# Kernel optimization log

Hardware: AMD Instinct MI355X
Metric: run time of the kernel (lower is better)

Reference implementation:

```python
import jax, jax.numpy as jnp
import numpy as np

HEADS = 16
D_MODEL = 1024


def setup_inputs() -> dict:
    key = jax.random.key(0)
    ks = jax.random.split(key, 12)
    B, S, D = 4, 2048, D_MODEL
    s = 1.0 / np.sqrt(D)
    return {
        "q": jax.random.normal(ks[0], (B, S, D), jnp.float32),
        "k": jax.random.normal(ks[1], (B, S, D), jnp.float32),
        "v": jax.random.normal(ks[2], (B, S, D), jnp.float32),
        "mask": jnp.ones((B, S, S), jnp.int32),
        "W_q": jax.random.normal(ks[3], (D, D), jnp.float32) * s,
        "b_q": jnp.zeros((D,), jnp.float32),
        "W_k": jax.random.normal(ks[4], (D, D), jnp.float32) * s,
        "b_k": jnp.zeros((D,), jnp.float32),
        "W_v": jax.random.normal(ks[5], (D, D), jnp.float32) * s,
        "b_v": jnp.zeros((D,), jnp.float32),
        "W_o": jax.random.normal(ks[6], (D, D), jnp.float32) * s,
        "b_o": jnp.zeros((D,), jnp.float32),
    }


def reference(q, k, v, mask, W_q, b_q, W_k, b_k, W_v, b_v, W_o, b_o):
    B, Sq, D = q.shape
    H = HEADS
    d_k = D // H
    # torch Linear: x @ W.T + b
    qh = (q @ W_q.T + b_q).reshape(B, Sq, H, d_k).transpose(0, 2, 1, 3)
    kh = (k @ W_k.T + b_k).reshape(B, -1, H, d_k).transpose(0, 2, 1, 3)
    vh = (v @ W_v.T + b_v).reshape(B, -1, H, d_k).transpose(0, 2, 1, 3)
    scores = jnp.einsum("bhqd,bhkd->bhqk", qh, kh) / jnp.sqrt(jnp.float32(d_k))
    scores = jnp.where(mask[:, None, :, :] == 0, -jnp.inf, scores)
    attn = jax.nn.softmax(scores, axis=-1)
    out = jnp.einsum("bhqk,bhkd->bhqd", attn, vh)
    out = out.transpose(0, 2, 1, 3).reshape(B, Sq, D)
    return out @ W_o.T + b_o
```

## Files before the change

### kernel.cpp

```cpp
#include <hip/hip_runtime.h>
#include <hip/hip_bf16.h>
#include <cmath>
#include <cstddef>

#define B_  4
#define S_  2048
#define D_  1024
#define H_  16
#define DK_ 64
#define M_  (B_*S_)
#define MB(x) ((size_t)(x) << 20)

typedef unsigned short u16;
typedef __attribute__((ext_vector_type(8))) short s16x8;
typedef __attribute__((ext_vector_type(8))) unsigned short u16x8;
typedef __attribute__((ext_vector_type(4))) unsigned short u16x4;
typedef __attribute__((ext_vector_type(4))) float f32x4;
typedef __attribute__((ext_vector_type(4))) unsigned int u32x4;
typedef __attribute__((ext_vector_type(2))) unsigned long long ull2;

typedef __attribute__((address_space(3))) char as3char;
typedef __attribute__((address_space(1))) const char as1char;

__device__ inline u16 f2bf(float f) {
  unsigned int u = __float_as_uint(f);
  u += 0x7fffu + ((u >> 16) & 1u);
  return (u16)(u >> 16);
}
__device__ inline float bf2f(u16 h) {
  return __uint_as_float(((unsigned int)h) << 16);
}

__device__ inline size_t tsw(int m, int k) {
  int row = m & 127, kk = k & 63;
  return ((size_t)((m >> 7) * 16 + (k >> 6)) << 14)
       + (size_t)(((row * 128 + (kk >> 3) * 16) ^ ((row & 7) << 4)) + (kk & 7) * 2);
}

__global__ __launch_bounds__(256)
void pack_mask(const int* __restrict__ mask, unsigned long long* __restrict__ Mp)
{
  int w    = blockIdx.x * 4 + (threadIdx.x >> 6);
  int lane = threadIdx.x & 63;
  int m = mask[(size_t)w * 64 + lane];
  unsigned long long bits = __ballot(m != 0);
  if (lane == 0) Mp[w] = bits;
}

__global__ __launch_bounds__(256)
void split_w_t(const float* __restrict__ W, u16* __restrict__ hi,
               u16* __restrict__ lo)
{
  int id = blockIdx.x * 256 + threadIdx.x;
  int n  = id >> 7;
  int k8 = (id & 127) << 3;
  const float* p = W + (size_t)n * 1024 + k8;
  float4 x0 = *(const float4*)p;
  float4 x1 = *(const float4*)(p + 4);
  float xs[8] = {x0.x, x0.y, x0.z, x0.w, x1.x, x1.y, x1.z, x1.w};
  u16x8 h, l;
#pragma unroll
  for (int e = 0; e < 8; ++e) {
    u16 hh = f2bf(xs[e]);
    h[e] = hh;
    l[e] = f2bf(xs[e] - bf2f(hh));
  }
  size_t byte = tsw(n, k8);
  *(u16x8*)((char*)hi + byte) = h;
  *(u16x8*)((char*)lo + byte) = l;
}

__global__ __launch_bounds__(256)
void cvt3(const float* __restrict__ a, const float* __restrict__ b,
          const float* __restrict__ c, u16* __restrict__ oa,
          u16* __restrict__ ob, u16* __restrict__ oc)
{
  const float* src = blockIdx.z == 0 ? a : (blockIdx.z == 1 ? b : c);
  u16*         dst = blockIdx.z == 0 ? oa : (blockIdx.z == 1 ? ob : oc);
  int id = blockIdx.x * 256 + threadIdx.x;
  int m  = id >> 7;
  int k8 = (id & 127) << 3;
  const float* p = src + (size_t)m * 1024 + k8;
  float4 x0 = *(const float4*)p;
  float4 x1 = *(const float4*)(p + 4);
  u16x8 px;
  px[0]=f2bf(x0.x); px[1]=f2bf(x0.y); px[2]=f2bf(x0.z); px[3]=f2bf(x0.w);
  px[4]=f2bf(x1.x); px[5]=f2bf(x1.y); px[6]=f2bf(x1.z); px[7]=f2bf(x1.w);
  *(u16x8*)((char*)dst + tsw(m, k8)) = px;
}

template<int MODE>
__global__ __launch_bounds__(256)
void proj_gemm_t(const u16* __restrict__ Xb, const u16* __restrict__ Wb,
                 const float* __restrict__ bias, u16* __restrict__ out,
                 float scale)
{
  __shared__ __align__(16) u16 smem[16384];
  char* const sX = (char*)smem;
  char* const sW = (char*)smem + 16384;

  const int tid  = threadIdx.x;
  const int lane = tid & 63, wid = tid >> 6;
  const int l15  = lane & 15, l4 = lane >> 4;
  const int wm = (wid >> 1) * 64, wn = (wid & 1) * 64;
  const int mb = blockIdx.x, nb = blockIdx.y;

  f32x4 acc[4][4];
#pragma unroll
  for (int i = 0; i < 4; ++i)
#pragma unroll
    for (int j = 0; j < 4; ++j)
      acc[i][j] = f32x4{0.f, 0.f, 0.f, 0.f};

  const char* xsrc = (const char*)Xb + ((size_t)(mb * 16) << 14) + wid * 4096 + lane * 16;
  const char* wsrc = (const char*)Wb + ((size_t)(nb * 16) << 14) + wid * 4096 + lane * 16;

  for (int kb = 0; kb < 16; ++kb) {
#pragma unroll
    for (int i = 0; i < 4; ++i) {
      __builtin_amdgcn_global_load_lds((const as1char*)(xsrc + i * 1024),
                                       (as3char*)(sX + wid * 4096 + i * 1024), 16, 0, 0);
      __builtin_amdgcn_global_load_lds((const as1char*)(wsrc + i * 1024),
                                       (as3char*)(sW + wid * 4096 + i * 1024), 16, 0, 0);
    }
    xsrc += 16384; wsrc += 16384;
    __syncthreads();

#pragma unroll
    for (int kc = 0; kc < 2; ++kc) {
      s16x8 af[4], bf[4];
#pragma unroll
      for (int i = 0; i < 4; ++i) {
        int ar = wm + i * 16 + l15;
        af[i] = *(const s16x8*)(sX + ((ar * 128 + kc * 64 + l4 * 16) ^ ((ar & 7) << 4)));
        int br = wn + i * 16 + l15;
        bf[i] = *(const s16x8*)(sW + ((br * 128 + kc * 64 + l4 * 16) ^ ((br & 7) << 4)));
      }
#pragma unroll
      for (int i = 0; i < 4; ++i)
#pragma unroll
        for (int j = 0; j < 4; ++j)
          acc[i][j] = __builtin_amdgcn_mfma_f32_16x16x32_bf16(af[i], bf[j], acc[i][j], 0, 0, 0);
    }
    __syncthreads();
  }

  float bj[4];
#pragma unroll
  for (int j = 0; j < 4; ++j) bj[j] = bias[nb * 128 + wn + j * 16 + l15];

#pragma unroll
  for (int i = 0; i < 4; ++i) {
#pragma unroll
    for (int r = 0; r < 4; ++r) {
      int mm = mb * 128 + wm + i * 16 + l4 * 4 + r;
      int bb = mm >> 11, s = mm & (S_ - 1);
#pragma unroll
      for (int j = 0; j < 4; ++j) {
        int n = nb * 128 + wn + j * 16 + l15;
        int hh = n >> 6, d = n & 63;
        u16 val = f2bf((acc[i][j][r] + bj[j]) * scale);
        if (MODE == 0)
          out[(((size_t)bb * H_ + hh) * S_ + s) * DK_ + d] = val;
        else
          out[(((size_t)bb * H_ + hh) * DK_ + d) * S_ + s] = val;
      }
    }
  }
}

__global__ __launch_bounds__(256)
void proj_out_t(const u16* __restrict__ Xhi, const u16* __restrict__ Xlo,
                const u16* __restrict__ Whi, const u16* __restrict__ Wlo,
                const float* __restrict__ bias, float* __restrict__ out)
{
  __shared__ __align__(16) u16 smem[32768];
  char* const sXh = (char*)smem;
  char* const sXl = (char*)smem + 16384;
  char* const sWh = (char*)smem + 32768;
  char* const sWl = (char*)smem + 49152;

  const int tid  = threadIdx.x;
  const int lane = tid & 63, wid = tid >> 6;
  const int l15  = lane & 15, l4 = lane >> 4;
  const int wm = (wid >> 1) * 64, wn = (wid & 1) * 64;
  const int mb = blockIdx.x, nb = blockIdx.y;

  f32x4 acc[4][4];
#pragma unroll
  for (int i = 0; i < 4; ++i)
#pragma unroll
    for (int j = 0; j < 4; ++j)
      acc[i][j] = f32x4{0.f, 0.f, 0.f, 0.f};

  const int toff = wid * 4096 + lane * 16;
  const char* xh = (const char*)Xhi + ((size_t)(mb * 16) << 14) + toff;
  const char* xl = (const char*)Xlo + ((size_t)(mb * 16) << 14) + toff;
  const char* wh = (const char*)Whi + ((size_t)(nb * 16) << 14) + toff;
  const char* wl = (const char*)Wlo + ((size_t)(nb * 16) << 14) + toff;

  for (int kb = 0; kb < 16; ++kb) {
#pragma unroll
    for (int i = 0; i < 4; ++i) {
      __builtin_amdgcn_global_load_lds((const as1char*)(xh + i * 1024),
                                       (as3char*)(sXh + wid * 4096 + i * 1024), 16, 0, 0);
      __builtin_amdgcn_global_load_lds((const as1char*)(xl + i * 1024),
                                       (as3char*)(sXl + wid * 4096 + i * 1024), 16, 0, 0);
      __builtin_amdgcn_global_load_lds((const as1char*)(wh + i * 1024),
                                       (as3char*)(sWh + wid * 4096 + i * 1024), 16, 0, 0);
      __builtin_amdgcn_global_load_lds((const as1char*)(wl + i * 1024),
                                       (as3char*)(sWl + wid * 4096 + i * 1024), 16, 0, 0);
    }
    xh += 16384; xl += 16384; wh += 16384; wl += 16384;
    __syncthreads();

#pragma unroll
    for (int kc = 0; kc < 2; ++kc) {
      s16x8 ah[4], al[4], bh[4], bl[4];
#pragma unroll
      for (int i = 0; i < 4; ++i) {
        int ar = wm + i * 16 + l15;
        int aoff = (ar * 128 + kc * 64 + l4 * 16) ^ ((ar & 7) << 4);
        ah[i] = *(const s16x8*)(sXh + aoff);
        al[i] = *(const s16x8*)(sXl + aoff);
        int br = wn + i * 16 + l15;
        int boff = (br * 128 + kc * 64 + l4 * 16) ^ ((br & 7) << 4);
        bh[i] = *(const s16x8*)(sWh + boff);
        bl[i] = *(const s16x8*)(sWl + boff);
      }
#pragma unroll
      for (int i = 0; i < 4; ++i)
#pragma unroll
        for (int j = 0; j < 4; ++j) {
          acc[i][j] = __builtin_amdgcn_mfma_f32_16x16x32_bf16(ah[i], bh[j], acc[i][j], 0, 0, 0);
          acc[i][j] = __builtin_amdgcn_mfma_f32_16x16x32_bf16(ah[i], bl[j], acc[i][j], 0, 0, 0);
          acc[i][j] = __builtin_amdgcn_mfma_f32_16x16x32_bf16(al[i], bh[j], acc[i][j], 0, 0, 0);
        }
    }
    __syncthreads();
  }

  float bj[4];
#pragma unroll
  for (int j = 0; j < 4; ++j) bj[j] = bias[nb * 128 + wn + j * 16 + l15];

#pragma unroll
  for (int i = 0; i < 4; ++i) {
#pragma unroll
    for (int r = 0; r < 4; ++r) {
      int mm = mb * 128 + wm + i * 16 + l4 * 4 + r;
#pragma unroll
      for (int j = 0; j < 4; ++j) {
        int n = nb * 128 + wn + j * 16 + l15;
        out[(size_t)mm * D_ + n] = acc[i][j][r] + bj[j];
      }
    }
  }
}

__global__ __launch_bounds__(512)
void flash_attn_mfma5(const u16* __restrict__ Qh, const u16* __restrict__ Kh,
                      const u16* __restrict__ Vt,
                      const unsigned long long* __restrict__ Mp,
                      u16* __restrict__ AOhi, u16* __restrict__ AOlo)
{
  __shared__ __align__(16) char smem[16896];
  char* const sK = smem;
  char* const sV = smem + 8192;

  const int tid  = threadIdx.x;
  const int lane = tid & 63, wid = tid >> 6;
  const int l15  = lane & 15, l4 = lane >> 4;

  const int bh = blockIdx.y;
  const int b  = bh >> 4, h = bh & 15;
  const int q0 = blockIdx.x * 128;
  const int qw = q0 + wid * 16;
  const int myq = qw + l15;

  const float L2E = 1.4426950408889634f;

  const u16* qbase = Qh + ((size_t)bh * S_ + myq) * DK_;
  s16x8 qf[2];
  qf[0] = *(const s16x8*)(qbase + l4 * 8);
  qf[1] = *(const s16x8*)(qbase + 32 + l4 * 8);

  const int srow = tid >> 3;
  const int sd8  = (tid & 7) * 8;
  const int kdst = (srow * 128 + (tid & 7) * 16) ^ ((srow & 7) << 4);
  const int vdst = srow * 136 + (((tid & 7) * 16) ^ (((srow >> 3) & 7) << 4));
  const u16* kg = Kh + (size_t)bh * S_ * DK_ + (size_t)srow * DK_ + sd8;
  const u16* vg = Vt + (size_t)bh * DK_ * S_ + (size_t)srow * S_ + sd8;

  const int kswz = (l15 & 7) << 4;
  const int kcol = l4 * 16;

  const unsigned long long* mrow = Mp + ((size_t)b * S_ + myq) * (S_ / 64);

  f32x4 o[4];
#pragma unroll
  for (int n = 0; n < 4; ++n) o[n] = f32x4{0.f, 0.f, 0.f, 0.f};
  float m_i = -INFINITY, l_i = 0.f;
  float ml2 = -1e30f * L2E;

  u16x8 kreg = *(const u16x8*)(kg);
  u16x8 vreg = *(const u16x8*)(vg);
  unsigned long long mb_next = mrow[0];

  for (int t = 0; t < S_ / 64; ++t) {
    __syncthreads();
    *(u16x8*)(sK + kdst) = kreg;
    *(u16x8*)(sV + vdst) = vreg;
    unsigned long long mbits = mb_next;
    __syncthreads();

    if (t + 1 < S_ / 64) {
      kreg = *(const u16x8*)(kg + (size_t)(t + 1) * 64 * DK_);
      vreg = *(const u16x8*)(vg + (size_t)(t + 1) * 64);
      mb_next = mrow[t + 1];
    }

    f32x4 sc[4];
#pragma unroll
    for (int n = 0; n < 4; ++n) {
      sc[n] = f32x4{0.f, 0.f, 0.f, 0.f};
#pragma unroll
      for (int kc = 0; kc < 2; ++kc) {
        int row = n * 16 + l15;
        s16x8 kf = *(const s16x8*)(sK + ((row * 128 + kc * 64 + kcol) ^ kswz));
        sc[n] = __builtin_amdgcn_mfma_f32_16x16x32_bf16(kf, qf[kc], sc[n], 0, 0, 0);
      }
    }

    float s[4][4];
    if (__all(mbits == 0xFFFFFFFFFFFFFFFFull)) {
#pragma unroll
      for (int n = 0; n < 4; ++n)
#pragma unroll
        for (int r = 0; r < 4; ++r) s[n][r] = sc[n][r];
    } else {
#pragma unroll
      for (int n = 0; n < 4; ++n) {
        unsigned mb2 = (unsigned)(mbits >> (n * 16 + l4 * 4)) & 15u;
#pragma unroll
        for (int r = 0; r < 4; ++r)
          s[n][r] = (mb2 >> r) & 1u ? sc[n][r] : -INFINITY;
      }
    }

    float mt = fmaxf(fmaxf(s[0][0], s[0][1]), fmaxf(s[0][2], s[0][3]));
#pragma unroll
    for (int n = 1; n < 4; ++n)
      mt = fmaxf(mt, fmaxf(fmaxf(s[n][0], s[n][1]), fmaxf(s[n][2], s[n][3])));
    mt = fmaxf(mt, __shfl_xor(mt, 16));
    mt = fmaxf(mt, __shfl_xor(mt, 32));

    if (!__all(mt - m_i <= 8.f)) {
      float mn = fmaxf(m_i, mt);
      float alpha = (m_i == -INFINITY) ? 0.f
                    : __builtin_amdgcn_exp2f((m_i - mn) * L2E);
      float ab[4];
#pragma unroll
      for (int r = 0; r < 4; ++r) ab[r] = __shfl(alpha, l4 * 4 + r);
#pragma unroll
      for (int n = 0; n < 4; ++n)
#pragma unroll
        for (int r = 0; r < 4; ++r) o[n][r] *= ab[r];
      l_i *= alpha;
      m_i = mn;
      ml2 = fmaxf(mn, -1e30f) * L2E;
    }

    float p[4][4];
    float rs = 0.f;
#pragma unroll
    for (int n = 0; n < 4; ++n)
#pragma unroll
      for (int r = 0; r < 4; ++r) {
        p[n][r] = __builtin_amdgcn_exp2f(fmaf(s[n][r], L2E, -ml2));
        rs += p[n][r];
      }
    rs += __shfl_xor(rs, 16);
    rs += __shfl_xor(rs, 32);
    l_i += rs;

    s16x8 pf[2];
#pragma unroll
    for (int kc = 0; kc < 2; ++kc) {
      unsigned r0, r1, r2, r3;
      asm("v_cvt_pk_bf16_f32 %0, %1, %2" : "=v"(r0) : "v"(p[2*kc][0]),   "v"(p[2*kc][1]));
      asm("v_cvt_pk_bf16_f32 %0, %1, %2" : "=v"(r1) : "v"(p[2*kc][2]),   "v"(p[2*kc][3]));
      asm("v_cvt_pk_bf16_f32 %0, %1, %2" : "=v"(r2) : "v"(p[2*kc+1][0]), "v"(p[2*kc+1][1]));
      asm("v_cvt_pk_bf16_f32 %0, %1, %2" : "=v"(r3) : "v"(p[2*kc+1][2]), "v"(p[2*kc+1][3]));
      u32x4 uu = {r0, r1, r2, r3};
      pf[kc] = __builtin_bit_cast(s16x8, uu);
    }

#pragma unroll
    for (int kc = 0; kc < 2; ++kc) {
      int k0b = kc * 64 + 8 * l4;
#pragma unroll
      for (int n = 0; n < 4; ++n) {
        int d    = n * 16 + l15;
        int rowb = d * 136;
        int swz  = ((d >> 3) & 7) << 4;
        ull2 uu;
        uu[0] = *(const unsigned long long*)(sV + rowb + (k0b ^ swz));
        uu[1] = *(const unsigned long long*)(sV + rowb + ((k0b + 32) ^ swz));
        s16x8 vf = __builtin_bit_cast(s16x8, uu);
        o[n] = __builtin_amdgcn_mfma_f32_16x16x32_bf16(pf[kc], vf, o[n], 0, 0, 0);
      }
    }
  }

  float linv[4];
#pragma unroll
  for (int r = 0; r < 4; ++r) {
    float lr = __shfl(l_i, l4 * 4 + r);
    linv[r] = lr > 0.f ? 1.f / lr : 0.f;
  }
#pragma unroll
  for (int n = 0; n < 4; ++n)
#pragma unroll
    for (int r = 0; r < 4; ++r) {
      float val = o[n][r] * linv[r];
      u16 hh = f2bf(val);
      int m = b * S_ + qw + l4 * 4 + r;
      int k = h * 64 + n * 16 + l15;
      size_t byte = tsw(m, k);
      *(u16*)((char*)AOhi + byte) = hh;
      *(u16*)((char*)AOlo + byte) = f2bf(val - bf2f(hh));
    }
}

extern "C" void kernel_launch(void* const* d_in, const int* in_sizes, int n_in,
                              void* d_out, int out_size, void* d_ws, size_t ws_size,
                              hipStream_t stream)
{
  const float* q    = (const float*)d_in[0];
  const float* k    = (const float*)d_in[1];
  const float* v    = (const float*)d_in[2];
  const int*   mask = (const int*)  d_in[3];
  const float* Wq   = (const float*)d_in[4];
  const float* bq   = (const float*)d_in[5];
  const float* Wk   = (const float*)d_in[6];
  const float* bk   = (const float*)d_in[7];
  const float* Wv   = (const float*)d_in[8];
  const float* bv   = (const float*)d_in[9];
  const float* Wo   = (const float*)d_in[10];
  const float* bo   = (const float*)d_in[11];
  float* out = (float*)d_out;

  char* ws = (char*)d_ws;
  u16* Qh   = (u16*)(ws);
  u16* Kh   = (u16*)(ws + MB(16));
  u16* Vt   = (u16*)(ws + MB(32));
  u16* AOhi = (u16*)(ws + MB(48));
  u16* AOlo = (u16*)(ws + MB(64));
  u16* Whi  = (u16*)(ws + MB(80));
  u16* Wlo  = (u16*)(ws + MB(82));
  unsigned long long* Mp = (unsigned long long*)(ws + MB(84));
  u16* kb2  = (u16*)(ws + MB(48));
  u16* qb2  = (u16*)(ws + MB(64));
  u16* vb2  = (u16*)(ws + MB(86));
  u16* Wqb  = (u16*)(ws + MB(102));
  u16* Wkb  = (u16*)(ws + MB(104));
  u16* Wvb  = (u16*)(ws + MB(106));

  dim3 tblk(256);

  cvt3<<<dim3(4096, 1, 3), tblk, 0, stream>>>(q, k, v, qb2, kb2, vb2);
  cvt3<<<dim3(512, 1, 3), tblk, 0, stream>>>(Wq, Wk, Wv, Wqb, Wkb, Wvb);
  pack_mask<<<dim3((B_ * S_ * (S_ / 64)) / 4), tblk, 0, stream>>>(mask, Mp);
  split_w_t<<<dim3(512), tblk, 0, stream>>>(Wo, Whi, Wlo);

  dim3 gproj(M_ / 128, D_ / 128);
  proj_gemm_t<0><<<gproj, tblk, 0, stream>>>(qb2, Wqb, bq, Qh, 0.125f);
  proj_gemm_t<0><<<gproj, tblk, 0, stream>>>(kb2, Wkb, bk, Kh, 1.0f);
  proj_gemm_t<1><<<gproj, tblk, 0, stream>>>(vb2, Wvb, bv, Vt, 1.0f);

  dim3 gattn(S_ / 128, B_ * H_);
  flash_attn_mfma5<<<gattn, dim3(512), 0, stream>>>(Qh, Kh, Vt, Mp, AOhi, AOlo);

  proj_out_t<<<gproj, tblk, 0, stream>>>(AOhi, AOlo, Whi, Wlo, bo, out);
}
```

Measured before the change: 301.1 us.

## Pre-swizzle K/V tile images and double-buffer attention with direct global-to-LDS loads

The K and V projection kernels now write tiles in the exact swizzled LDS image the attention kernel expects. The attention kernel can then stream each 8 KB tile straight into shared memory with global_load_lds and double-buffer two K/V stages, cutting one barrier per tile. The V fragment read becomes a single 16-byte LDS load instead of two 8-byte loads, and workgroups are remapped so blocks sharing a batch-head run closer together. The cost is double the LDS per block, which may lower occupancy, and more complex scattered stores in the projection epilogue.

```diff
diff --git a/kernel.cpp b/kernel.cpp
--- a/kernel.cpp
+++ b/kernel.cpp
@@ -17,7 +17,6 @@
 typedef __attribute__((ext_vector_type(4))) unsigned short u16x4;
 typedef __attribute__((ext_vector_type(4))) float f32x4;
 typedef __attribute__((ext_vector_type(4))) unsigned int u32x4;
-typedef __attribute__((ext_vector_type(2))) unsigned long long ull2;
 
 typedef __attribute__((address_space(3))) char as3char;
 typedef __attribute__((address_space(1))) const char as1char;
@@ -160,10 +159,20 @@
         int n = nb * 128 + wn + j * 16 + l15;
         int hh = n >> 6, d = n & 63;
         u16 val = f2bf((acc[i][j][r] + bj[j]) * scale);
-        if (MODE == 0)
+        if (MODE == 0) {
           out[(((size_t)bb * H_ + hh) * S_ + s) * DK_ + d] = val;
-        else
-          out[(((size_t)bb * H_ + hh) * DK_ + d) * S_ + s] = val;
+        } else if (MODE == 2) {
+          size_t base = (((size_t)bb * H_ + hh) * 32 + (s >> 6)) * 8192;
+          int r2 = s & 63;
+          *(u16*)((char*)out + base
+                  + (((r2 * 128 + (d >> 3) * 16) ^ ((r2 & 7) << 4)) + (d & 7) * 2)) = val;
+        } else {
+          size_t base = (((size_t)bb * H_ + hh) * 32 + (s >> 6)) * 8192;
+          int kk2 = s & 63;
+          int slot = ((kk2 >> 5) * 4 + ((kk2 >> 2) & 3) + d) & 7;
+          *(u16*)((char*)out + base
+                  + d * 128 + slot * 16 + ((kk2 >> 4) & 1) * 8 + (kk2 & 3) * 2) = val;
+        }
       }
     }
   }
@@ -259,22 +268,26 @@
 }
 
 __global__ __launch_bounds__(512)
-void flash_attn_mfma5(const u16* __restrict__ Qh, const u16* __restrict__ Kh,
-                      const u16* __restrict__ Vt,
+void flash_attn_mfma6(const u16* __restrict__ Qh, const char* __restrict__ Kimg,
+                      const char* __restrict__ Vimg,
                       const unsigned long long* __restrict__ Mp,
                       u16* __restrict__ AOhi, u16* __restrict__ AOlo)
 {
-  __shared__ __align__(16) char smem[16896];
-  char* const sK = smem;
-  char* const sV = smem + 8192;
+  __shared__ __align__(16) char smem[32768];
+  char* const sK0 = smem;
+  char* const sV0 = smem + 8192;
+  char* const sK1 = smem + 16384;
+  char* const sV1 = smem + 24576;
 
   const int tid  = threadIdx.x;
   const int lane = tid & 63, wid = tid >> 6;
   const int l15  = lane & 15, l4 = lane >> 4;
 
-  const int bh = blockIdx.y;
-  const int b  = bh >> 4, h = bh & 15;
-  const int q0 = blockIdx.x * 128;
+  const int wgid = blockIdx.x + (blockIdx.y << 4);
+  const int bh   = (wgid & 7) * 8 + (wgid >> 7);
+  const int qt   = (wgid >> 3) & 15;
+  const int b = bh >> 4, h = bh & 15;
+  const int q0 = qt * 128;
   const int qw = q0 + wid * 16;
   const int myq = qw + l15;
 
@@ -285,15 +298,14 @@
   qf[0] = *(const s16x8*)(qbase + l4 * 8);
   qf[1] = *(const s16x8*)(qbase + 32 + l4 * 8);
 
-  const int srow = tid >> 3;
-  const int sd8  = (tid & 7) * 8;
-  const int kdst = (srow * 128 + (tid & 7) * 16) ^ ((srow & 7) << 4);
-  const int vdst = srow * 136 + (((tid & 7) * 16) ^ (((srow >> 3) & 7) << 4));
-  const u16* kg = Kh + (size_t)bh * S_ * DK_ + (size_t)srow * DK_ + sd8;
-  const u16* vg = Vt + (size_t)bh * DK_ * S_ + (size_t)srow * S_ + sd8;
+  const char* kimg = Kimg + (size_t)bh * 32 * 8192 + tid * 16;
+  const char* vimg = Vimg + (size_t)bh * 32 * 8192 + tid * 16;
+  const int ldst = wid * 1024;
 
   const int kswz = (l15 & 7) << 4;
   const int kcol = l4 * 16;
+  const int vs0  = ((l4 + l15) & 7) * 16;
+  const int vs1  = ((4 + l4 + l15) & 7) * 16;
 
   const unsigned long long* mrow = Mp + ((size_t)b * S_ + myq) * (S_ / 64);
 
@@ -303,23 +315,15 @@
   float m_i = -INFINITY, l_i = 0.f;
   float ml2 = -1e30f * L2E;
 
-  u16x8 kreg = *(const u16x8*)(kg);
-  u16x8 vreg = *(const u16x8*)(vg);
-  unsigned long long mb_next = mrow[0];
-
-  for (int t = 0; t < S_ / 64; ++t) {
-    __syncthreads();
-    *(u16x8*)(sK + kdst) = kreg;
-    *(u16x8*)(sV + vdst) = vreg;
-    unsigned long long mbits = mb_next;
-    __syncthreads();
-
-    if (t + 1 < S_ / 64) {
-      kreg = *(const u16x8*)(kg + (size_t)(t + 1) * 64 * DK_);
-      vreg = *(const u16x8*)(vg + (size_t)(t + 1) * 64);
-      mb_next = mrow[t + 1];
-    }
-
+  auto stage = [&](char* sKd, char* sVd, int t) {
+    __builtin_amdgcn_global_load_lds((const as1char*)(kimg + (size_t)t * 8192),
+                                     (as3char*)(sKd + ldst), 16, 0, 0);
+    __builtin_amdgcn_global_load_lds((const as1char*)(vimg + (size_t)t * 8192),
+                                     (as3char*)(sVd + ldst), 16, 0, 0);
+  };
+
+  auto compute_tile = [&](const char* sKc, const char* sVc,
+                          unsigned long long mbits) {
     f32x4 sc[4];
 #pragma unroll
     for (int n = 0; n < 4; ++n) {
@@ -327,31 +331,25 @@
 #pragma unroll
       for (int kc = 0; kc < 2; ++kc) {
         int row = n * 16 + l15;
-        s16x8 kf = *(const s16x8*)(sK + ((row * 128 + kc * 64 + kcol) ^ kswz));
+        s16x8 kf = *(const s16x8*)(sKc + ((row * 128 + kc * 64 + kcol) ^ kswz));
         sc[n] = __builtin_amdgcn_mfma_f32_16x16x32_bf16(kf, qf[kc], sc[n], 0, 0, 0);
       }
     }
 
-    float s[4][4];
-    if (__all(mbits == 0xFFFFFFFFFFFFFFFFull)) {
-#pragma unroll
-      for (int n = 0; n < 4; ++n)
-#pragma unroll
-        for (int r = 0; r < 4; ++r) s[n][r] = sc[n][r];
-    } else {
+    if (!__all(mbits == 0xFFFFFFFFFFFFFFFFull)) {
 #pragma unroll
       for (int n = 0; n < 4; ++n) {
         unsigned mb2 = (unsigned)(mbits >> (n * 16 + l4 * 4)) & 15u;
 #pragma unroll
         for (int r = 0; r < 4; ++r)
-          s[n][r] = (mb2 >> r) & 1u ? sc[n][r] : -INFINITY;
-      }
-    }
-
-    float mt = fmaxf(fmaxf(s[0][0], s[0][1]), fmaxf(s[0][2], s[0][3]));
+          if (!((mb2 >> r) & 1u)) sc[n][r] = -INFINITY;
+      }
+    }
+
+    float mt = fmaxf(fmaxf(sc[0][0], sc[0][1]), fmaxf(sc[0][2], sc[0][3]));
 #pragma unroll
     for (int n = 1; n < 4; ++n)
-      mt = fmaxf(mt, fmaxf(fmaxf(s[n][0], s[n][1]), fmaxf(s[n][2], s[n][3])));
+      mt = fmaxf(mt, fmaxf(fmaxf(sc[n][0], sc[n][1]), fmaxf(sc[n][2], sc[n][3])));
     mt = fmaxf(mt, __shfl_xor(mt, 16));
     mt = fmaxf(mt, __shfl_xor(mt, 32));
 
@@ -377,7 +375,7 @@
     for (int n = 0; n < 4; ++n)
 #pragma unroll
       for (int r = 0; r < 4; ++r) {
-        p[n][r] = __builtin_amdgcn_exp2f(fmaf(s[n][r], L2E, -ml2));
+        p[n][r] = __builtin_amdgcn_exp2f(fmaf(sc[n][r], L2E, -ml2));
         rs += p[n][r];
       }
     rs += __shfl_xor(rs, 16);
@@ -397,20 +395,30 @@
     }
 
 #pragma unroll
-    for (int kc = 0; kc < 2; ++kc) {
-      int k0b = kc * 64 + 8 * l4;
+    for (int kc = 0; kc < 2; ++kc)
 #pragma unroll
       for (int n = 0; n < 4; ++n) {
-        int d    = n * 16 + l15;
-        int rowb = d * 136;
-        int swz  = ((d >> 3) & 7) << 4;
-        ull2 uu;
-        uu[0] = *(const unsigned long long*)(sV + rowb + (k0b ^ swz));
-        uu[1] = *(const unsigned long long*)(sV + rowb + ((k0b + 32) ^ swz));
-        s16x8 vf = __builtin_bit_cast(s16x8, uu);
+        s16x8 vf = *(const s16x8*)(sVc + n * 2048 + l15 * 128 + (kc ? vs1 : vs0));
         o[n] = __builtin_amdgcn_mfma_f32_16x16x32_bf16(pf[kc], vf, o[n], 0, 0, 0);
       }
-    }
+  };
+
+  unsigned long long mb_next = mrow[0];
+  stage(sK0, sV0, 0);
+  __syncthreads();
+
+  for (int t = 0; t < S_ / 64; t += 2) {
+    if (t + 1 < S_ / 64) stage(sK1, sV1, t + 1);
+    unsigned long long mbits = mb_next;
+    if (t + 1 < S_ / 64) mb_next = mrow[t + 1];
+    compute_tile(sK0, sV0, mbits);
+    __syncthreads();
+
+    if (t + 2 < S_ / 64) stage(sK0, sV0, t + 2);
+    mbits = mb_next;
+    if (t + 2 < S_ / 64) mb_next = mrow[t + 2];
+    compute_tile(sK1, sV1, mbits);
+    __syncthreads();
   }
 
   float linv[4];
@@ -452,13 +460,13 @@
   float* out = (float*)d_out;
 
   char* ws = (char*)d_ws;
-  u16* Qh   = (u16*)(ws);
-  u16* Kh   = (u16*)(ws + MB(16));
-  u16* Vt   = (u16*)(ws + MB(32));
-  u16* AOhi = (u16*)(ws + MB(48));
-  u16* AOlo = (u16*)(ws + MB(64));
-  u16* Whi  = (u16*)(ws + MB(80));
-  u16* Wlo  = (u16*)(ws + MB(82));
+  u16*  Qh   = (u16*)(ws);
+  char* Kimg = ws + MB(16);
+  char* Vimg = ws + MB(32);
+  u16*  AOhi = (u16*)(ws + MB(48));
+  u16*  AOlo = (u16*)(ws + MB(64));
+  u16*  Whi  = (u16*)(ws + MB(80));
+  u16*  Wlo  = (u16*)(ws + MB(82));
   unsigned long long* Mp = (unsigned long long*)(ws + MB(84));
   u16* kb2  = (u16*)(ws + MB(48));
   u16* qb2  = (u16*)(ws + MB(64));
@@ -476,11 +484,11 @@
 
   dim3 gproj(M_ / 128, D_ / 128);
   proj_gemm_t<0><<<gproj, tblk, 0, stream>>>(qb2, Wqb, bq, Qh, 0.125f);
-  proj_gemm_t<0><<<gproj, tblk, 0, stream>>>(kb2, Wkb, bk, Kh, 1.0f);
-  proj_gemm_t<1><<<gproj, tblk, 0, stream>>>(vb2, Wvb, bv, Vt, 1.0f);
+  proj_gemm_t<2><<<gproj, tblk, 0, stream>>>(kb2, Wkb, bk, (u16*)Kimg, 1.0f);
+  proj_gemm_t<1><<<gproj, tblk, 0, stream>>>(vb2, Wvb, bv, (u16*)Vimg, 1.0f);
 
   dim3 gattn(S_ / 128, B_ * H_);
-  flash_attn_mfma5<<<gattn, dim3(512), 0, stream>>>(Qh, Kh, Vt, Mp, AOhi, AOlo);
+  flash_attn_mfma6<<<gattn, dim3(512), 0, stream>>>(Qh, Kimg, Vimg, Mp, AOhi, AOlo);
 
   proj_out_t<<<gproj, tblk, 0, stream>>>(AOhi, AOlo, Whi, Wlo, bo, out);
 }
```

Measured after the change: 287.5 us. -4.5%, faster.
